# Optimization experiments

Hardware: AMD Instinct MI355X
Metric: run time of the kernel (lower is better)

The kernel has to match this reference:

```python
import jax, jax.numpy as jnp
import numpy as np

N_NODES = 10000
N_EDGES = 640000
D_FEAT = 128


def setup_inputs() -> dict:
    key = jax.random.key(0)
    k1, k2, k3, k4 = jax.random.split(key, 4)
    feat = jax.random.normal(k1, (N_NODES, D_FEAT), dtype=jnp.float32)
    src = jax.random.randint(k2, (N_EDGES,), 0, N_NODES, dtype=jnp.int32)
    dst = jax.random.randint(k3, (N_EDGES,), 0, N_NODES, dtype=jnp.int32)
    W = jax.random.normal(k4, (D_FEAT, D_FEAT), dtype=jnp.float32) / np.sqrt(D_FEAT).astype(np.float32)
    b = jnp.zeros((D_FEAT,), dtype=jnp.float32)
    return {"feat": feat, "W": W, "b": b, "src": src, "dst": dst}


def reference(feat, W, b, src, dst):
    eps = jnp.float32(0.0)  # init_eps=0, learn_eps=False (buffer)
    n = feat.shape[0]
    # message passing: copy_u('h','m') + sum reducer -> neigh[i] = sum_{j->i} h_j
    h_src = feat[src]                                   # [E, D] gather
    neigh = jax.ops.segment_sum(h_src, dst, num_segments=n)  # [N, D] scatter-add
    rst = (1.0 + eps) * feat + neigh
    # apply_func: Linear(D, D)
    rst = rst @ W + b
    # per-edge score: e = sum(h_src * tanh(h_dst), axis=1)
    e = jnp.sum(h_src * jnp.tanh(feat[dst]), axis=1)    # [E]
    # edge_softmax: softmax over edges grouped by destination node
    m = jax.ops.segment_max(e, dst, num_segments=n)     # [N]
    e_exp = jnp.exp(e - m[dst])
    denom = jax.ops.segment_sum(e_exp, dst, num_segments=n)  # [N]
    e_soft = e_exp / denom[dst]
    return rst, e_soft
```

## Files before the change

### kernel.cpp

```cpp
#include <hip/hip_runtime.h>
#include <hip/hip_bf16.h>
#include <math.h>

#define N_NODES 10000
#define N_EDGES 640000
#define D_FEAT  128
#define SLOT    128
#define MAXDEG  128


__global__ void scatter_build(const int* __restrict__ src,
                              const int* __restrict__ dst,
                              int* __restrict__ cnt,
                              unsigned short* __restrict__ slot_us,
                              int* __restrict__ pos_by_edge) {
    int i0 = (blockIdx.x * 256 + threadIdx.x) * 4;
    int4 s4 = *(const int4*)&src[i0];
    int4 d4 = *(const int4*)&dst[i0];
    int p0 = atomicAdd(&cnt[d4.x << 4], 1);
    int p1 = atomicAdd(&cnt[d4.y << 4], 1);
    int p2 = atomicAdd(&cnt[d4.z << 4], 1);
    int p3 = atomicAdd(&cnt[d4.w << 4], 1);
    int4 q;
    q.x = d4.x * SLOT + p0;
    q.y = d4.y * SLOT + p1;
    q.z = d4.z * SLOT + p2;
    q.w = d4.w * SLOT + p3;
    slot_us[q.x] = (unsigned short)s4.x;
    slot_us[q.y] = (unsigned short)s4.y;
    slot_us[q.z] = (unsigned short)s4.z;
    slot_us[q.w] = (unsigned short)s4.w;
    *(int4*)&pos_by_edge[i0] = q;
}

__global__ void fused_node(const float* __restrict__ feat,
                           const int* __restrict__ cnt,
                           const unsigned short* __restrict__ slot_us,
                           float* __restrict__ e_slot,
                           float* __restrict__ x_out) {
    __shared__ float t_sh[4][D_FEAT];
    __shared__ float e_sh[4][MAXDEG];
    int wv = threadIdx.x >> 6;
    int lane = threadIdx.x & 63;
    int node = blockIdx.x * 4 + wv;
    if (node >= N_NODES) return;

    int g = lane >> 4;
    int l = lane & 15;

    int deg = cnt[node << 4];
    int dm = (deg > 0) ? deg - 1 : 0;
    unsigned base = (unsigned)node * SLOT;

    float2 fd2 = ((const float2*)(feat + (size_t)node * D_FEAT))[lane];
    ((float2*)&t_sh[wv][0])[lane] = make_float2(tanhf(fd2.x), tanhf(fd2.y));
    float4 t0 = ((const float4*)&t_sh[wv][0])[l * 2];
    float4 t1 = ((const float4*)&t_sh[wv][0])[l * 2 + 1];

    int m0 = (int)slot_us[base + min(lane, dm)];
    int m1 = (int)slot_us[base + min(64 + lane, dm)];

    float4 acc0 = make_float4(0.f, 0.f, 0.f, 0.f);
    float4 acc1 = make_float4(0.f, 0.f, 0.f, 0.f);

    int nsteps = (deg + 7) >> 3;

    float4 Va0, Va1, Va2, Va3;
    #define LOAD_STEP(T, V0, V1, V2, V3)                                      \
        {                                                                     \
            int m_ = ((T) < 8) ? m0 : m1;                                     \
            int s0_ = __shfl(m_, ((T) * 8 + g) & 63, 64);                     \
            int s1_ = __shfl(m_, ((T) * 8 + 4 + g) & 63, 64);                 \
            const float4* r0_ = (const float4*)(feat + (size_t)s0_ * D_FEAT) + l * 2; \
            const float4* r1_ = (const float4*)(feat + (size_t)s1_ * D_FEAT) + l * 2; \
            V0 = r0_[0]; V1 = r0_[1]; V2 = r1_[0]; V3 = r1_[1];               \
        }

    if (nsteps > 0) LOAD_STEP(0, Va0, Va1, Va2, Va3);

    for (int t = 0; t < nsteps; ++t) {
        float4 Vb0 = Va0, Vb1 = Va1, Vb2 = Va2, Vb3 = Va3;
        if (t + 1 < nsteps) LOAD_STEP(t + 1, Vb0, Vb1, Vb2, Vb3);

        int i0 = t * 8 + g;
        int i1 = i0 + 4;
        if (((t + 1) << 3) <= deg) {
            acc0.x += Va0.x + Va2.x; acc0.y += Va0.y + Va2.y;
            acc0.z += Va0.z + Va2.z; acc0.w += Va0.w + Va2.w;
            acc1.x += Va1.x + Va3.x; acc1.y += Va1.y + Va3.y;
            acc1.z += Va1.z + Va3.z; acc1.w += Va1.w + Va3.w;
            float d0 = Va0.x * t0.x + Va0.y * t0.y + Va0.z * t0.z + Va0.w * t0.w
                     + Va1.x * t1.x + Va1.y * t1.y + Va1.z * t1.z + Va1.w * t1.w;
            float d1 = Va2.x * t0.x + Va2.y * t0.y + Va2.z * t0.z + Va2.w * t0.w
                     + Va3.x * t1.x + Va3.y * t1.y + Va3.z * t1.z + Va3.w * t1.w;
            #pragma unroll
            for (int off = 1; off <= 8; off <<= 1) {
                d0 += __shfl_xor(d0, off, 64);
                d1 += __shfl_xor(d1, off, 64);
            }
            if (l == 0) {
                e_sh[wv][i0] = d0;
                e_sh[wv][i1] = d1;
            }
        } else {
            bool a0 = i0 < deg, a1 = i1 < deg;
            if (!a0) {
                Va0 = make_float4(0.f, 0.f, 0.f, 0.f);
                Va1 = make_float4(0.f, 0.f, 0.f, 0.f);
            }
            if (!a1) {
                Va2 = make_float4(0.f, 0.f, 0.f, 0.f);
                Va3 = make_float4(0.f, 0.f, 0.f, 0.f);
            }
            acc0.x += Va0.x + Va2.x; acc0.y += Va0.y + Va2.y;
            acc0.z += Va0.z + Va2.z; acc0.w += Va0.w + Va2.w;
            acc1.x += Va1.x + Va3.x; acc1.y += Va1.y + Va3.y;
            acc1.z += Va1.z + Va3.z; acc1.w += Va1.w + Va3.w;
            float d0 = Va0.x * t0.x + Va0.y * t0.y + Va0.z * t0.z + Va0.w * t0.w
                     + Va1.x * t1.x + Va1.y * t1.y + Va1.z * t1.z + Va1.w * t1.w;
            float d1 = Va2.x * t0.x + Va2.y * t0.y + Va2.z * t0.z + Va2.w * t0.w
                     + Va3.x * t1.x + Va3.y * t1.y + Va3.z * t1.z + Va3.w * t1.w;
            #pragma unroll
            for (int off = 1; off <= 8; off <<= 1) {
                d0 += __shfl_xor(d0, off, 64);
                d1 += __shfl_xor(d1, off, 64);
            }
            if (a0 && l == 0) e_sh[wv][i0] = d0;
            if (a1 && l == 0) e_sh[wv][i1] = d1;
        }
        Va0 = Vb0; Va1 = Vb1; Va2 = Vb2; Va3 = Vb3;
    }
    #undef LOAD_STEP

    #pragma unroll
    for (int off = 16; off <= 32; off <<= 1) {
        acc0.x += __shfl_xor(acc0.x, off, 64);
        acc0.y += __shfl_xor(acc0.y, off, 64);
        acc0.z += __shfl_xor(acc0.z, off, 64);
        acc0.w += __shfl_xor(acc0.w, off, 64);
        acc1.x += __shfl_xor(acc1.x, off, 64);
        acc1.y += __shfl_xor(acc1.y, off, 64);
        acc1.z += __shfl_xor(acc1.z, off, 64);
        acc1.w += __shfl_xor(acc1.w, off, 64);
    }

    float2 mp = (g == 0) ? make_float2(acc0.x, acc0.y)
              : (g == 1) ? make_float2(acc0.z, acc0.w)
              : (g == 2) ? make_float2(acc1.x, acc1.y)
              :            make_float2(acc1.z, acc1.w);
    int p2 = l * 4 + g;
    float2 fn = ((const float2*)(feat + (size_t)node * D_FEAT))[p2];
    ((float2*)(x_out + (size_t)node * D_FEAT))[p2] =
        make_float2(mp.x + fn.x, mp.y + fn.y);

    float mx = -INFINITY;
    for (int i = lane; i < deg; i += 64) mx = fmaxf(mx, e_sh[wv][i]);
    #pragma unroll
    for (int off = 32; off; off >>= 1)
        mx = fmaxf(mx, __shfl_xor(mx, off, 64));

    float sum = 0.f;
    for (int i = lane; i < deg; i += 64) {
        float ex = expf(e_sh[wv][i] - mx);
        e_sh[wv][i] = ex;
        sum += ex;
    }
    #pragma unroll
    for (int off = 32; off; off >>= 1)
        sum += __shfl_xor(sum, off, 64);

    float inv = 1.0f / sum;
    for (int i = lane; i < deg; i += 64)
        e_slot[base + i] = e_sh[wv][i] * inv;
}

__global__ void gemm_and_edge(float* __restrict__ io,
                              const float* __restrict__ W,
                              const float* __restrict__ b,
                              const int* __restrict__ pos_by_edge,
                              const float* __restrict__ e_slot,
                              float* __restrict__ out_e) {
    if (blockIdx.x >= 625) {
        int i4 = ((blockIdx.x - 625) * 256 + threadIdx.x) * 4;
        int4 p = *(const int4*)&pos_by_edge[i4];
        float4 r;
        r.x = e_slot[p.x];
        r.y = e_slot[p.y];
        r.z = e_slot[p.z];
        r.w = e_slot[p.w];
        *(float4*)&out_e[i4] = r;
        return;
    }

    __shared__ float xst[D_FEAT][20];
    int rbase = blockIdx.x * 16;

    for (int i = threadIdx.x; i < 16 * D_FEAT; i += 256) {
        int r = i >> 7, c = i & 127;
        xst[c][r] = io[(size_t)(rbase + r) * D_FEAT + c];
    }
    __syncthreads();

    int tc = threadIdx.x & 63;
    int rh = threadIdx.x >> 6;
    float a00 = 0.f, a01 = 0.f, a10 = 0.f, a11 = 0.f;
    float a20 = 0.f, a21 = 0.f, a30 = 0.f, a31 = 0.f;

    for (int k = 0; k < D_FEAT; ++k) {
        float2 xa = *(const float2*)&xst[k][rh * 4];
        float2 xb = *(const float2*)&xst[k][rh * 4 + 2];
        float2 w  = *(const float2*)&W[(size_t)k * D_FEAT + tc * 2];
        a00 += xa.x * w.x; a01 += xa.x * w.y;
        a10 += xa.y * w.x; a11 += xa.y * w.y;
        a20 += xb.x * w.x; a21 += xb.x * w.y;
        a30 += xb.y * w.x; a31 += xb.y * w.y;
    }
    __syncthreads();

    float2 bias = *(const float2*)&b[tc * 2];
    int rw = rbase + rh * 4;
    ((float2*)&io[(size_t)(rw + 0) * D_FEAT])[tc] = make_float2(a00 + bias.x, a01 + bias.y);
    ((float2*)&io[(size_t)(rw + 1) * D_FEAT])[tc] = make_float2(a10 + bias.x, a11 + bias.y);
    ((float2*)&io[(size_t)(rw + 2) * D_FEAT])[tc] = make_float2(a20 + bias.x, a21 + bias.y);
    ((float2*)&io[(size_t)(rw + 3) * D_FEAT])[tc] = make_float2(a30 + bias.x, a31 + bias.y);
}

extern "C" void kernel_launch(void* const* d_in, const int* in_sizes, int n_in,
                              void* d_out, int out_size, void* d_ws, size_t ws_size,
                              hipStream_t stream) {
    const float* feat = (const float*)d_in[0];
    const float* W    = (const float*)d_in[1];
    const float* b    = (const float*)d_in[2];
    const int*   src  = (const int*)d_in[3];
    const int*   dst  = (const int*)d_in[4];

    float* out_rst = (float*)d_out;
    float* out_e   = (float*)d_out + (size_t)N_NODES * D_FEAT;

    char* ws = (char*)d_ws;
    int*            cnt         = (int*)(ws + 0);
    unsigned short* slot_us     = (unsigned short*)(ws + 640000);
    float*          e_slot      = (float*)(ws + 3200000);
    int*            pos_by_edge = (int*)(ws + 8320000);

    hipMemsetAsync(cnt, 0, 640000, stream);

    scatter_build<<<N_EDGES / 4 / 256, 256, 0, stream>>>(src, dst, cnt, slot_us, pos_by_edge);

    fused_node<<<(N_NODES + 3) / 4, 256, 0, stream>>>(feat, cnt, slot_us, e_slot, out_rst);

    gemm_and_edge<<<1250, 256, 0, stream>>>(out_rst, W, b, pos_by_edge, e_slot, out_e);
}
```

Baseline: 141.0 us.

## Merge memset, scatter, node and GEMM stages into one cooperative persistent kernel

Replaces the memset plus three kernel launches with a single cooperative kernel of 512 persistent blocks that runs each stage in a grid-stride loop, separated by grid-wide syncs. The goal is to remove launch and inter-kernel gaps. The original kernels stay as a fallback if the cooperative launch fails. In exchange it adds three grid barriers and reduces parallelism per stage: the scatter loses its int4 vectorization, and the node stage is limited to 512 blocks with launch_bounds(256,2).

```diff
diff --git a/kernel.cpp b/kernel.cpp
--- a/kernel.cpp
+++ b/kernel.cpp
@@ -1,13 +1,243 @@
 #include <hip/hip_runtime.h>
+#include <hip/hip_cooperative_groups.h>
 #include <hip/hip_bf16.h>
 #include <math.h>
+
+namespace cg = cooperative_groups;
 
 #define N_NODES 10000
 #define N_EDGES 640000
 #define D_FEAT  128
 #define SLOT    128
 #define MAXDEG  128
-
+#define NBLK    512
+#define NTHR    (NBLK * 256)
+
+
+__device__ __forceinline__ void fused_node_body(
+        const float* __restrict__ feat, int deg, unsigned base,
+        const unsigned short* __restrict__ slot_us,
+        float* __restrict__ e_slot, float* __restrict__ io,
+        int node, int wv, int lane,
+        float (*t_sh)[D_FEAT], float (*e_sh)[MAXDEG]) {
+    int g = lane >> 4;
+    int l = lane & 15;
+    int dm = (deg > 0) ? deg - 1 : 0;
+
+    float2 fd2 = ((const float2*)(feat + (size_t)node * D_FEAT))[lane];
+    ((float2*)&t_sh[wv][0])[lane] = make_float2(tanhf(fd2.x), tanhf(fd2.y));
+    float4 t0 = ((const float4*)&t_sh[wv][0])[l * 2];
+    float4 t1 = ((const float4*)&t_sh[wv][0])[l * 2 + 1];
+
+    int m0 = (int)slot_us[base + min(lane, dm)];
+    int m1 = (int)slot_us[base + min(64 + lane, dm)];
+
+    float4 acc0 = make_float4(0.f, 0.f, 0.f, 0.f);
+    float4 acc1 = make_float4(0.f, 0.f, 0.f, 0.f);
+
+    int nsteps = (deg + 7) >> 3;
+
+    float4 Va0, Va1, Va2, Va3;
+    #define LOAD_STEP(T, V0, V1, V2, V3)                                      \
+        {                                                                     \
+            int m_ = ((T) < 8) ? m0 : m1;                                     \
+            int s0_ = __shfl(m_, ((T) * 8 + g) & 63, 64);                     \
+            int s1_ = __shfl(m_, ((T) * 8 + 4 + g) & 63, 64);                 \
+            const float4* r0_ = (const float4*)(feat + (size_t)s0_ * D_FEAT) + l * 2; \
+            const float4* r1_ = (const float4*)(feat + (size_t)s1_ * D_FEAT) + l * 2; \
+            V0 = r0_[0]; V1 = r0_[1]; V2 = r1_[0]; V3 = r1_[1];               \
+        }
+
+    if (nsteps > 0) LOAD_STEP(0, Va0, Va1, Va2, Va3);
+
+    for (int t = 0; t < nsteps; ++t) {
+        float4 Vb0 = Va0, Vb1 = Va1, Vb2 = Va2, Vb3 = Va3;
+        if (t + 1 < nsteps) LOAD_STEP(t + 1, Vb0, Vb1, Vb2, Vb3);
+
+        int i0 = t * 8 + g;
+        int i1 = i0 + 4;
+        if (((t + 1) << 3) <= deg) {
+            acc0.x += Va0.x + Va2.x; acc0.y += Va0.y + Va2.y;
+            acc0.z += Va0.z + Va2.z; acc0.w += Va0.w + Va2.w;
+            acc1.x += Va1.x + Va3.x; acc1.y += Va1.y + Va3.y;
+            acc1.z += Va1.z + Va3.z; acc1.w += Va1.w + Va3.w;
+            float d0 = Va0.x * t0.x + Va0.y * t0.y + Va0.z * t0.z + Va0.w * t0.w
+                     + Va1.x * t1.x + Va1.y * t1.y + Va1.z * t1.z + Va1.w * t1.w;
+            float d1 = Va2.x * t0.x + Va2.y * t0.y + Va2.z * t0.z + Va2.w * t0.w
+                     + Va3.x * t1.x + Va3.y * t1.y + Va3.z * t1.z + Va3.w * t1.w;
+            #pragma unroll
+            for (int off = 1; off <= 8; off <<= 1) {
+                d0 += __shfl_xor(d0, off, 64);
+                d1 += __shfl_xor(d1, off, 64);
+            }
+            if (l == 0) {
+                e_sh[wv][i0] = d0;
+                e_sh[wv][i1] = d1;
+            }
+        } else {
+            bool a0 = i0 < deg, a1 = i1 < deg;
+            if (!a0) {
+                Va0 = make_float4(0.f, 0.f, 0.f, 0.f);
+                Va1 = make_float4(0.f, 0.f, 0.f, 0.f);
+            }
+            if (!a1) {
+                Va2 = make_float4(0.f, 0.f, 0.f, 0.f);
+                Va3 = make_float4(0.f, 0.f, 0.f, 0.f);
+            }
+            acc0.x += Va0.x + Va2.x; acc0.y += Va0.y + Va2.y;
+            acc0.z += Va0.z + Va2.z; acc0.w += Va0.w + Va2.w;
+            acc1.x += Va1.x + Va3.x; acc1.y += Va1.y + Va3.y;
+            acc1.z += Va1.z + Va3.z; acc1.w += Va1.w + Va3.w;
+            float d0 = Va0.x * t0.x + Va0.y * t0.y + Va0.z * t0.z + Va0.w * t0.w
+                     + Va1.x * t1.x + Va1.y * t1.y + Va1.z * t1.z + Va1.w * t1.w;
+            float d1 = Va2.x * t0.x + Va2.y * t0.y + Va2.z * t0.z + Va2.w * t0.w
+                     + Va3.x * t1.x + Va3.y * t1.y + Va3.z * t1.z + Va3.w * t1.w;
+            #pragma unroll
+            for (int off = 1; off <= 8; off <<= 1) {
+                d0 += __shfl_xor(d0, off, 64);
+                d1 += __shfl_xor(d1, off, 64);
+            }
+            if (a0 && l == 0) e_sh[wv][i0] = d0;
+            if (a1 && l == 0) e_sh[wv][i1] = d1;
+        }
+        Va0 = Vb0; Va1 = Vb1; Va2 = Vb2; Va3 = Vb3;
+    }
+    #undef LOAD_STEP
+
+    #pragma unroll
+    for (int off = 16; off <= 32; off <<= 1) {
+        acc0.x += __shfl_xor(acc0.x, off, 64);
+        acc0.y += __shfl_xor(acc0.y, off, 64);
+        acc0.z += __shfl_xor(acc0.z, off, 64);
+        acc0.w += __shfl_xor(acc0.w, off, 64);
+        acc1.x += __shfl_xor(acc1.x, off, 64);
+        acc1.y += __shfl_xor(acc1.y, off, 64);
+        acc1.z += __shfl_xor(acc1.z, off, 64);
+        acc1.w += __shfl_xor(acc1.w, off, 64);
+    }
+
+    float2 mp = (g == 0) ? make_float2(acc0.x, acc0.y)
+              : (g == 1) ? make_float2(acc0.z, acc0.w)
+              : (g == 2) ? make_float2(acc1.x, acc1.y)
+              :            make_float2(acc1.z, acc1.w);
+    int p2 = l * 4 + g;
+    float2 fn = ((const float2*)(feat + (size_t)node * D_FEAT))[p2];
+    ((float2*)(io + (size_t)node * D_FEAT))[p2] =
+        make_float2(mp.x + fn.x, mp.y + fn.y);
+
+    float mx = -INFINITY;
+    for (int i = lane; i < deg; i += 64) mx = fmaxf(mx, e_sh[wv][i]);
+    #pragma unroll
+    for (int off = 32; off; off >>= 1)
+        mx = fmaxf(mx, __shfl_xor(mx, off, 64));
+
+    float sum = 0.f;
+    for (int i = lane; i < deg; i += 64) {
+        float ex = expf(e_sh[wv][i] - mx);
+        e_sh[wv][i] = ex;
+        sum += ex;
+    }
+    #pragma unroll
+    for (int off = 32; off; off >>= 1)
+        sum += __shfl_xor(sum, off, 64);
+
+    float inv = 1.0f / sum;
+    for (int i = lane; i < deg; i += 64)
+        e_slot[base + i] = e_sh[wv][i] * inv;
+}
+
+__device__ __forceinline__ void gemm_tile_body(
+        float* __restrict__ io, const float* __restrict__ W,
+        const float* __restrict__ b, int tile, float (*xst)[20]) {
+    int rbase = tile * 16;
+    for (int i = threadIdx.x; i < 16 * D_FEAT; i += 256) {
+        int r = i >> 7, cc = i & 127;
+        xst[cc][r] = io[(size_t)(rbase + r) * D_FEAT + cc];
+    }
+    __syncthreads();
+
+    int tc = threadIdx.x & 63;
+    int rh = threadIdx.x >> 6;
+    float a00 = 0.f, a01 = 0.f, a10 = 0.f, a11 = 0.f;
+    float a20 = 0.f, a21 = 0.f, a30 = 0.f, a31 = 0.f;
+
+    for (int k = 0; k < D_FEAT; ++k) {
+        float2 xa = *(const float2*)&xst[k][rh * 4];
+        float2 xb = *(const float2*)&xst[k][rh * 4 + 2];
+        float2 w  = *(const float2*)&W[(size_t)k * D_FEAT + tc * 2];
+        a00 += xa.x * w.x; a01 += xa.x * w.y;
+        a10 += xa.y * w.x; a11 += xa.y * w.y;
+        a20 += xb.x * w.x; a21 += xb.x * w.y;
+        a30 += xb.y * w.x; a31 += xb.y * w.y;
+    }
+    __syncthreads();
+
+    float2 bias = *(const float2*)&b[tc * 2];
+    int rw = rbase + rh * 4;
+    ((float2*)&io[(size_t)(rw + 0) * D_FEAT])[tc] = make_float2(a00 + bias.x, a01 + bias.y);
+    ((float2*)&io[(size_t)(rw + 1) * D_FEAT])[tc] = make_float2(a10 + bias.x, a11 + bias.y);
+    ((float2*)&io[(size_t)(rw + 2) * D_FEAT])[tc] = make_float2(a20 + bias.x, a21 + bias.y);
+    ((float2*)&io[(size_t)(rw + 3) * D_FEAT])[tc] = make_float2(a30 + bias.x, a31 + bias.y);
+}
+
+__global__ __launch_bounds__(256, 2)
+void mega(const float* __restrict__ feat,
+          const float* __restrict__ W,
+          const float* __restrict__ b,
+          const int* __restrict__ src,
+          const int* __restrict__ dst,
+          int* __restrict__ cnt,
+          unsigned short* __restrict__ slot_us,
+          float* __restrict__ e_slot,
+          int* __restrict__ pos_by_edge,
+          float* __restrict__ io,
+          float* __restrict__ out_e) {
+    cg::grid_group grid = cg::this_grid();
+    const int tid = blockIdx.x * 256 + threadIdx.x;
+
+    __shared__ float t_sh[4][D_FEAT];
+    __shared__ float e_sh[4][MAXDEG];
+    __shared__ float xst[D_FEAT][20];
+
+    for (int i = tid; i < N_NODES * 16; i += NTHR) cnt[i] = 0;
+    grid.sync();
+
+    for (int i = tid; i < N_EDGES; i += NTHR) {
+        int d = dst[i];
+        int s = src[i];
+        int pos = atomicAdd(&cnt[d << 4], 1);
+        int idx = d * SLOT + pos;
+        slot_us[idx] = (unsigned short)s;
+        pos_by_edge[i] = idx;
+    }
+    grid.sync();
+
+    {
+        int wv = threadIdx.x >> 6;
+        int lane = threadIdx.x & 63;
+        for (int node = blockIdx.x * 4 + wv; node < N_NODES; node += NBLK * 4) {
+            int deg = cnt[node << 4];
+            fused_node_body(feat, deg, (unsigned)node * SLOT, slot_us,
+                            e_slot, io, node, wv, lane, t_sh, e_sh);
+        }
+    }
+    grid.sync();
+
+    for (int c = blockIdx.x; c < 1250; c += NBLK) {
+        if (c >= 625) {
+            int i4 = ((c - 625) * 256 + threadIdx.x) * 4;
+            int4 p = *(const int4*)&pos_by_edge[i4];
+            float4 r;
+            r.x = e_slot[p.x];
+            r.y = e_slot[p.y];
+            r.z = e_slot[p.z];
+            r.w = e_slot[p.w];
+            *(float4*)&out_e[i4] = r;
+            continue;
+        }
+        gemm_tile_body(io, W, b, c, xst);
+    }
+}
 
 __global__ void scatter_build(const int* __restrict__ src,
                               const int* __restrict__ dst,
@@ -33,145 +263,20 @@
     *(int4*)&pos_by_edge[i0] = q;
 }
 
-__global__ void fused_node(const float* __restrict__ feat,
-                           const int* __restrict__ cnt,
-                           const unsigned short* __restrict__ slot_us,
-                           float* __restrict__ e_slot,
-                           float* __restrict__ x_out) {
+__global__ void fused_node_k(const float* __restrict__ feat,
+                             const int* __restrict__ cnt,
+                             const unsigned short* __restrict__ slot_us,
+                             float* __restrict__ e_slot,
+                             float* __restrict__ io) {
     __shared__ float t_sh[4][D_FEAT];
     __shared__ float e_sh[4][MAXDEG];
     int wv = threadIdx.x >> 6;
     int lane = threadIdx.x & 63;
     int node = blockIdx.x * 4 + wv;
     if (node >= N_NODES) return;
-
-    int g = lane >> 4;
-    int l = lane & 15;
-
     int deg = cnt[node << 4];
-    int dm = (deg > 0) ? deg - 1 : 0;
-    unsigned base = (unsigned)node * SLOT;
-
-    float2 fd2 = ((const float2*)(feat + (size_t)node * D_FEAT))[lane];
-    ((float2*)&t_sh[wv][0])[lane] = make_float2(tanhf(fd2.x), tanhf(fd2.y));
-    float4 t0 = ((const float4*)&t_sh[wv][0])[l * 2];
-    float4 t1 = ((const float4*)&t_sh[wv][0])[l * 2 + 1];
-
-    int m0 = (int)slot_us[base + min(lane, dm)];
-    int m1 = (int)slot_us[base + min(64 + lane, dm)];
-
-    float4 acc0 = make_float4(0.f, 0.f, 0.f, 0.f);
-    float4 acc1 = make_float4(0.f, 0.f, 0.f, 0.f);
-
-    int nsteps = (deg + 7) >> 3;
-
-    float4 Va0, Va1, Va2, Va3;
-    #define LOAD_STEP(T, V0, V1, V2, V3)                                      \
-        {                                                                     \
-            int m_ = ((T) < 8) ? m0 : m1;                                     \
-            int s0_ = __shfl(m_, ((T) * 8 + g) & 63, 64);                     \
-            int s1_ = __shfl(m_, ((T) * 8 + 4 + g) & 63, 64);                 \
-            const float4* r0_ = (const float4*)(feat + (size_t)s0_ * D_FEAT) + l * 2; \
-            const float4* r1_ = (const float4*)(feat + (size_t)s1_ * D_FEAT) + l * 2; \
-            V0 = r0_[0]; V1 = r0_[1]; V2 = r1_[0]; V3 = r1_[1];               \
-        }
-
-    if (nsteps > 0) LOAD_STEP(0, Va0, Va1, Va2, Va3);
-
-    for (int t = 0; t < nsteps; ++t) {
-        float4 Vb0 = Va0, Vb1 = Va1, Vb2 = Va2, Vb3 = Va3;
-        if (t + 1 < nsteps) LOAD_STEP(t + 1, Vb0, Vb1, Vb2, Vb3);
-
-        int i0 = t * 8 + g;
-        int i1 = i0 + 4;
-        if (((t + 1) << 3) <= deg) {
-            acc0.x += Va0.x + Va2.x; acc0.y += Va0.y + Va2.y;
-            acc0.z += Va0.z + Va2.z; acc0.w += Va0.w + Va2.w;
-            acc1.x += Va1.x + Va3.x; acc1.y += Va1.y + Va3.y;
-            acc1.z += Va1.z + Va3.z; acc1.w += Va1.w + Va3.w;
-            float d0 = Va0.x * t0.x + Va0.y * t0.y + Va0.z * t0.z + Va0.w * t0.w
-                     + Va1.x * t1.x + Va1.y * t1.y + Va1.z * t1.z + Va1.w * t1.w;
-            float d1 = Va2.x * t0.x + Va2.y * t0.y + Va2.z * t0.z + Va2.w * t0.w
-                     + Va3.x * t1.x + Va3.y * t1.y + Va3.z * t1.z + Va3.w * t1.w;
-            #pragma unroll
-            for (int off = 1; off <= 8; off <<= 1) {
-                d0 += __shfl_xor(d0, off, 64);
-                d1 += __shfl_xor(d1, off, 64);
-            }
-            if (l == 0) {
-                e_sh[wv][i0] = d0;
-                e_sh[wv][i1] = d1;
-            }
-        } else {
-            bool a0 = i0 < deg, a1 = i1 < deg;
-            if (!a0) {
-                Va0 = make_float4(0.f, 0.f, 0.f, 0.f);
-                Va1 = make_float4(0.f, 0.f, 0.f, 0.f);
-            }
-            if (!a1) {
-                Va2 = make_float4(0.f, 0.f, 0.f, 0.f);
-                Va3 = make_float4(0.f, 0.f, 0.f, 0.f);
-            }
-            acc0.x += Va0.x + Va2.x; acc0.y += Va0.y + Va2.y;
-            acc0.z += Va0.z + Va2.z; acc0.w += Va0.w + Va2.w;
-            acc1.x += Va1.x + Va3.x; acc1.y += Va1.y + Va3.y;
-            acc1.z += Va1.z + Va3.z; acc1.w += Va1.w + Va3.w;
-            float d0 = Va0.x * t0.x + Va0.y * t0.y + Va0.z * t0.z + Va0.w * t0.w
-                     + Va1.x * t1.x + Va1.y * t1.y + Va1.z * t1.z + Va1.w * t1.w;
-            float d1 = Va2.x * t0.x + Va2.y * t0.y + Va2.z * t0.z + Va2.w * t0.w
-                     + Va3.x * t1.x + Va3.y * t1.y + Va3.z * t1.z + Va3.w * t1.w;
-            #pragma unroll
-            for (int off = 1; off <= 8; off <<= 1) {
-                d0 += __shfl_xor(d0, off, 64);
-                d1 += __shfl_xor(d1, off, 64);
-            }
-            if (a0 && l == 0) e_sh[wv][i0] = d0;
-            if (a1 && l == 0) e_sh[wv][i1] = d1;
-        }
-        Va0 = Vb0; Va1 = Vb1; Va2 = Vb2; Va3 = Vb3;
-    }
-    #undef LOAD_STEP
-
-    #pragma unroll
-    for (int off = 16; off <= 32; off <<= 1) {
-        acc0.x += __shfl_xor(acc0.x, off, 64);
-        acc0.y += __shfl_xor(acc0.y, off, 64);
-        acc0.z += __shfl_xor(acc0.z, off, 64);
-        acc0.w += __shfl_xor(acc0.w, off, 64);
-        acc1.x += __shfl_xor(acc1.x, off, 64);
-        acc1.y += __shfl_xor(acc1.y, off, 64);
-        acc1.z += __shfl_xor(acc1.z, off, 64);
-        acc1.w += __shfl_xor(acc1.w, off, 64);
-    }
-
-    float2 mp = (g == 0) ? make_float2(acc0.x, acc0.y)
-              : (g == 1) ? make_float2(acc0.z, acc0.w)
-              : (g == 2) ? make_float2(acc1.x, acc1.y)
-              :            make_float2(acc1.z, acc1.w);
-    int p2 = l * 4 + g;
-    float2 fn = ((const float2*)(feat + (size_t)node * D_FEAT))[p2];
-    ((float2*)(x_out + (size_t)node * D_FEAT))[p2] =
-        make_float2(mp.x + fn.x, mp.y + fn.y);
-
-    float mx = -INFINITY;
-    for (int i = lane; i < deg; i += 64) mx = fmaxf(mx, e_sh[wv][i]);
-    #pragma unroll
-    for (int off = 32; off; off >>= 1)
-        mx = fmaxf(mx, __shfl_xor(mx, off, 64));
-
-    float sum = 0.f;
-    for (int i = lane; i < deg; i += 64) {
-        float ex = expf(e_sh[wv][i] - mx);
-        e_sh[wv][i] = ex;
-        sum += ex;
-    }
-    #pragma unroll
-    for (int off = 32; off; off >>= 1)
-        sum += __shfl_xor(sum, off, 64);
-
-    float inv = 1.0f / sum;
-    for (int i = lane; i < deg; i += 64)
-        e_slot[base + i] = e_sh[wv][i] * inv;
+    fused_node_body(feat, deg, (unsigned)node * SLOT, slot_us,
+                    e_slot, io, node, wv, lane, t_sh, e_sh);
 }
 
 __global__ void gemm_and_edge(float* __restrict__ io,
@@ -180,6 +285,7 @@
                               const int* __restrict__ pos_by_edge,
                               const float* __restrict__ e_slot,
                               float* __restrict__ out_e) {
+    __shared__ float xst[D_FEAT][20];
     if (blockIdx.x >= 625) {
         int i4 = ((blockIdx.x - 625) * 256 + threadIdx.x) * 4;
         int4 p = *(const int4*)&pos_by_edge[i4];
@@ -191,38 +297,7 @@
         *(float4*)&out_e[i4] = r;
         return;
     }
-
-    __shared__ float xst[D_FEAT][20];
-    int rbase = blockIdx.x * 16;
-
-    for (int i = threadIdx.x; i < 16 * D_FEAT; i += 256) {
-        int r = i >> 7, c = i & 127;
-        xst[c][r] = io[(size_t)(rbase + r) * D_FEAT + c];
-    }
-    __syncthreads();
-
-    int tc = threadIdx.x & 63;
-    int rh = threadIdx.x >> 6;
-    float a00 = 0.f, a01 = 0.f, a10 = 0.f, a11 = 0.f;
-    float a20 = 0.f, a21 = 0.f, a30 = 0.f, a31 = 0.f;
-
-    for (int k = 0; k < D_FEAT; ++k) {
-        float2 xa = *(const float2*)&xst[k][rh * 4];
-        float2 xb = *(const float2*)&xst[k][rh * 4 + 2];
-        float2 w  = *(const float2*)&W[(size_t)k * D_FEAT + tc * 2];
-        a00 += xa.x * w.x; a01 += xa.x * w.y;
-        a10 += xa.y * w.x; a11 += xa.y * w.y;
-        a20 += xb.x * w.x; a21 += xb.x * w.y;
-        a30 += xb.y * w.x; a31 += xb.y * w.y;
-    }
-    __syncthreads();
-
-    float2 bias = *(const float2*)&b[tc * 2];
-    int rw = rbase + rh * 4;
-    ((float2*)&io[(size_t)(rw + 0) * D_FEAT])[tc] = make_float2(a00 + bias.x, a01 + bias.y);
-    ((float2*)&io[(size_t)(rw + 1) * D_FEAT])[tc] = make_float2(a10 + bias.x, a11 + bias.y);
-    ((float2*)&io[(size_t)(rw + 2) * D_FEAT])[tc] = make_float2(a20 + bias.x, a21 + bias.y);
-    ((float2*)&io[(size_t)(rw + 3) * D_FEAT])[tc] = make_float2(a30 + bias.x, a31 + bias.y);
+    gemm_tile_body(io, W, b, blockIdx.x, xst);
 }
 
 extern "C" void kernel_launch(void* const* d_in, const int* in_sizes, int n_in,
@@ -243,11 +318,15 @@
     float*          e_slot      = (float*)(ws + 3200000);
     int*            pos_by_edge = (int*)(ws + 8320000);
 
-    hipMemsetAsync(cnt, 0, 640000, stream);
-
-    scatter_build<<<N_EDGES / 4 / 256, 256, 0, stream>>>(src, dst, cnt, slot_us, pos_by_edge);
-
-    fused_node<<<(N_NODES + 3) / 4, 256, 0, stream>>>(feat, cnt, slot_us, e_slot, out_rst);
-
-    gemm_and_edge<<<1250, 256, 0, stream>>>(out_rst, W, b, pos_by_edge, e_slot, out_e);
-}
+    void* args[] = {(void*)&feat, (void*)&W, (void*)&b, (void*)&src, (void*)&dst,
+                    (void*)&cnt, (void*)&slot_us, (void*)&e_slot,
+                    (void*)&pos_by_edge, (void*)&out_rst, (void*)&out_e};
+    hipError_t err = hipLaunchCooperativeKernel((void*)mega, dim3(NBLK), dim3(256),
+                                                args, 0, stream);
+    if (err != hipSuccess) {
+        hipMemsetAsync(cnt, 0, 640000, stream);
+        scatter_build<<<N_EDGES / 4 / 256, 256, 0, stream>>>(src, dst, cnt, slot_us, pos_by_edge);
+        fused_node_k<<<(N_NODES + 3) / 4, 256, 0, stream>>>(feat, cnt, slot_us, e_slot, out_rst);
+        gemm_and_edge<<<1250, 256, 0, stream>>>(out_rst, W, b, pos_by_edge, e_slot, out_e);
+    }
+}
```

Measured after the change: 325.1 us. 2.31x slower.
